# Optimization experiments

Measured on AMD Instinct MI355X. Metric: run time of the kernel, lower is better.

## Reference

```python
import jax, jax.numpy as jnp
import numpy as np

INPUT_SIZE = 128
HID = 64
B, T = 256, 1024

def setup_inputs() -> dict:
    key = jax.random.key(0)
    ks = jax.random.split(key, 12)
    s1 = 1.0 / np.sqrt(HID)
    def u(k, shape):
        return jax.random.uniform(k, shape, jnp.float32, -s1, s1)
    return {
        "x": jax.random.normal(ks[0], (B, T, INPUT_SIZE), jnp.float32),
        "w_ih0": u(ks[1], (4 * HID, INPUT_SIZE)),
        "w_hh0": u(ks[2], (4 * HID, HID)),
        "b_ih0": u(ks[3], (4 * HID,)),
        "b_hh0": u(ks[4], (4 * HID,)),
        "w_ih1": u(ks[5], (4 * HID, HID)),
        "w_hh1": u(ks[6], (4 * HID, HID)),
        "b_ih1": u(ks[7], (4 * HID,)),
        "b_hh1": u(ks[8], (4 * HID,)),
        "w_out": u(ks[9], (1, HID)),
        "b_out": u(ks[10], (1,)),
    }

def _lstm(x, w_ih, w_hh, b_ih, b_hh):
    # x: [B, T, I] -> h sequence [B, T, H]; PyTorch gate order i, f, g, o
    Bb = x.shape[0]
    H = w_hh.shape[1]
    # precompute input contribution for all timesteps (one big GEMM)
    xg = jnp.einsum('bti,gi->btg', x, w_ih) + b_ih + b_hh  # [B, T, 4H]
    def step(carry, g_t):
        h, c = carry
        g = g_t + h @ w_hh.T  # [B, 4H]
        i, f, gg, o = jnp.split(g, 4, axis=-1)
        i = jax.nn.sigmoid(i)
        f = jax.nn.sigmoid(f)
        gg = jnp.tanh(gg)
        o = jax.nn.sigmoid(o)
        c = f * c + i * gg
        h = o * jnp.tanh(c)
        return (h, c), h
    init = (jnp.zeros((Bb, H), x.dtype), jnp.zeros((Bb, H), x.dtype))
    _, hs = jax.lax.scan(step, init, jnp.swapaxes(xg, 0, 1))  # [T, B, H]
    return jnp.swapaxes(hs, 0, 1)

def reference(x, w_ih0, w_hh0, b_ih0, b_hh0, w_ih1, w_hh1, b_ih1, b_hh1, w_out, b_out):
    h1 = _lstm(x, w_ih0, w_hh0, b_ih0, b_hh0)   # [B, T, H]
    h2 = _lstm(h1, w_ih1, w_hh1, b_ih1, b_hh1)  # [B, T, H]
    logits = jnp.einsum('bth,oh->bto', h2, w_out) + b_out  # [B, T, 1]
    return jax.nn.sigmoid(logits)
```

## Files before the change

kernel.cpp:

```cpp
#include <hip/hip_runtime.h>

#define BB 256
#define TT 1024
#define II 128
#define HH 64
#define BT (BB * TT)

typedef _Float16 h2 __attribute__((ext_vector_type(2)));
typedef _Float16 half8 __attribute__((ext_vector_type(8)));
typedef float f32x4 __attribute__((ext_vector_type(4)));
typedef unsigned int uint;
typedef unsigned short ushort;

#define BC(u) __builtin_bit_cast(h2, (uint)(u))
#define MFMA16(a, b, c) __builtin_amdgcn_mfma_f32_16x16x32_f16((a), (b), (c), 0, 0, 0)
#define SIG(v) __builtin_amdgcn_rcpf(1.0f + __expf(-(v)))
#define TNH(v) (1.0f - 2.0f * __builtin_amdgcn_rcpf(1.0f + __expf(2.0f * (v))))

#define BAR() asm volatile("s_waitcnt lgkmcnt(0)\n\ts_barrier" ::: "memory")

__device__ __forceinline__ uint pk2(float a, float b) {
    h2 h; h[0] = (_Float16)a; h[1] = (_Float16)b;
    return __builtin_bit_cast(uint, h);
}

__global__ __launch_bounds__(256)
void xg_mfma(const float* __restrict__ x, const float* __restrict__ w_ih0,
             ushort* __restrict__ xg)
{
    __shared__ __align__(16) _Float16 xt[64][136];
    __shared__ __align__(16) _Float16 wt[128][136];
    const int tid = threadIdx.x, lane = tid & 63, wv = tid >> 6;
    const int bt0 = blockIdx.x * 64;
    {
        const int row = tid >> 2, q = (tid & 3) * 32;
        const float4* src = (const float4*)(x + (size_t)(bt0 + row) * II + q);
        _Float16* dst = &xt[row][q];
        #pragma unroll
        for (int i = 0; i < 8; ++i) {
            float4 v = src[i];
            dst[4*i+0]=(_Float16)v.x; dst[4*i+1]=(_Float16)v.y;
            dst[4*i+2]=(_Float16)v.z; dst[4*i+3]=(_Float16)v.w;
        }
    }
    for (int nh = 0; nh < 2; ++nh) {
        __syncthreads();
        {
            const int n = tid >> 1, kh = (tid & 1) * 64;
            const int flatn = nh * 128 + n;
            const int srcrow = (flatn & 3) * 64 + (flatn >> 2);
            const float4* src = (const float4*)(w_ih0 + (size_t)srcrow * II + kh);
            _Float16* dst = &wt[n][kh];
            #pragma unroll
            for (int i = 0; i < 16; ++i) {
                float4 v = src[i];
                dst[4*i+0]=(_Float16)v.x; dst[4*i+1]=(_Float16)v.y;
                dst[4*i+2]=(_Float16)v.z; dst[4*i+3]=(_Float16)v.w;
            }
        }
        __syncthreads();
        const int m = wv * 16 + (lane & 15);
        const int kf = (lane >> 4) * 8;
        half8 a0 = *(const half8*)&xt[m][ 0 + kf];
        half8 a1 = *(const half8*)&xt[m][32 + kf];
        half8 a2 = *(const half8*)&xt[m][64 + kf];
        half8 a3 = *(const half8*)&xt[m][96 + kf];
        #pragma unroll
        for (int nt = 0; nt < 8; ++nt) {
            const int nloc = nt * 16 + (lane & 15);
            half8 b0 = *(const half8*)&wt[nloc][ 0 + kf];
            half8 b1 = *(const half8*)&wt[nloc][32 + kf];
            half8 b2 = *(const half8*)&wt[nloc][64 + kf];
            half8 b3 = *(const half8*)&wt[nloc][96 + kf];
            f32x4 acc = {0.f, 0.f, 0.f, 0.f};
            acc = MFMA16(a0, b0, acc); acc = MFMA16(a1, b1, acc);
            acc = MFMA16(a2, b2, acc); acc = MFMA16(a3, b3, acc);
            const int colg = nh * 128 + nt * 16 + (lane & 15);
            const int jj = colg >> 2, gg = colg & 3;
            const int r0 = wv * 16 + (lane >> 4) * 4;
            const int bloc = bt0 >> 10;
            const int tb = (bt0 & 1023) + r0;
            ushort* dst = xg + ((size_t)(bloc * 64 + jj) << 12) + gg;
            #pragma unroll
            for (int r = 0; r < 4; ++r) {
                _Float16 hv = (_Float16)acc[r];
                dst[(size_t)(tb + r) * 4] = __builtin_bit_cast(ushort, hv);
            }
        }
    }
}

__global__ __launch_bounds__(192) __attribute__((amdgpu_waves_per_eu(1, 1)))
void lstm2_core(const float* __restrict__ w_hh0,
                const float* __restrict__ b_ih0, const float* __restrict__ b_hh0,
                const float* __restrict__ w_ih1, const float* __restrict__ w_hh1,
                const float* __restrict__ b_ih1, const float* __restrict__ b_hh1,
                const ushort* __restrict__ xg, ushort* __restrict__ h1g)
{
    const int bb = blockIdx.x;
    const int w  = threadIdx.x >> 6;
    const int j  = threadIdx.x & 63;
    const int qq = j >> 4, cc = j & 15;

    __shared__ __align__(16) uint  h0buf[8][32];
    __shared__ __align__(16) uint  h1buf[32];
    __shared__ __align__(16) float zbuf[8][64][4];

    const float* Wsel = (w == 0) ? w_hh0 : (w == 1) ? w_ih1 : w_hh1;
    uint4 Bf[16][2];
    #pragma unroll
    for (int t = 0; t < 16; ++t) {
        const int row = (t & 3) * 64 + (t >> 2) * 16 + cc;
        const float* rp = Wsel + (size_t)row * 64 + qq * 8;
        #pragma unroll
        for (int kh = 0; kh < 2; ++kh) {
            const float* p = rp + kh * 32;
            uint4 v;
            v.x = pk2(p[0], p[1]); v.y = pk2(p[2], p[3]);
            v.z = pk2(p[4], p[5]); v.w = pk2(p[6], p[7]);
            Bf[t][kh] = v;
        }
    }

    float bI = 0.f, bF = 0.f, bG = 0.f, bO = 0.f;
    if (w == 0) {
        bI = b_ih0[j]       + b_hh0[j];
        bF = b_ih0[64 + j]  + b_hh0[64 + j];
        bG = b_ih0[128 + j] + b_hh0[128 + j];
        bO = b_ih0[192 + j] + b_hh0[192 + j];
    } else if (w == 2) {
        bI = b_ih1[j]       + b_hh1[j];
        bF = b_ih1[64 + j]  + b_hh1[64 + j];
        bG = b_ih1[128 + j] + b_hh1[128 + j];
        bO = b_ih1[192 + j] + b_hh1[192 + j];
    }

    float cst = 0.0f;
    const ushort* xb = xg + ((size_t)(bb * 64 + j) << 12);
    ushort* h1b = h1g + (size_t)bb * TT * 64 + j;

    const f32x4 ZR4 = {0.f, 0.f, 0.f, 0.f};
    const int qlo = qq & 1, qhi = qq >> 1;

    half8 af0 = {0,0,0,0,0,0,0,0}, af1 = {0,0,0,0,0,0,0,0};
    f32x4 zr = {0.f, 0.f, 0.f, 0.f};
    uint4 q0 = {0,0,0,0}, q1 = {0,0,0,0};
    if (w == 0) {
        q0 = *(const uint4*)(xb);
        q1 = *(const uint4*)(xb + 8);
    }

#define LDAF(SRC) { const char* hb_ = (const char*)(SRC); \
    af0 = *(const half8*)(hb_ + (qq << 4)); \
    af1 = *(const half8*)(hb_ + 64 + (qq << 4)); }

#define GEMV16(SI, SF, SG, SO) { \
    f32x4 D[16]; \
    _Pragma("unroll") \
    for (int t = 0; t < 16; ++t) { \
        f32x4 d_ = MFMA16(af0, __builtin_bit_cast(half8, Bf[t][0]), ZR4); \
        D[t] = MFMA16(af1, __builtin_bit_cast(half8, Bf[t][1]), d_); } \
    { float a_, b_; \
      a_ = qlo ? D[ 4][0] : D[ 0][0]; b_ = qlo ? D[12][0] : D[ 8][0]; SI = qhi ? b_ : a_; \
      a_ = qlo ? D[ 5][0] : D[ 1][0]; b_ = qlo ? D[13][0] : D[ 9][0]; SF = qhi ? b_ : a_; \
      a_ = qlo ? D[ 6][0] : D[ 2][0]; b_ = qlo ? D[14][0] : D[10][0]; SG = qhi ? b_ : a_; \
      a_ = qlo ? D[ 7][0] : D[ 3][0]; b_ = qlo ? D[15][0] : D[11][0]; SO = qhi ? b_ : a_; } }

#define PSTEP(KK, XLO, XHI) \
    if ((KK) < TT) { \
        float si, sf, sg, so; \
        GEMV16(si, sf, sg, so) \
        h2 xlo = BC(XLO), xhi = BC(XHI); \
        si += bI + (float)xlo[0]; sf += bF + (float)xlo[1]; \
        sg += bG + (float)xhi[0]; so += bO + (float)xhi[1]; \
        float ii = SIG(si), ff = SIG(sf), gg = TNH(sg), oo = SIG(so); \
        cst = fmaf(ff, cst, ii * gg); \
        float hval = oo * TNH(cst); \
        ((_Float16*)&h0buf[(KK) & 7][0])[j] = (_Float16)hval; \
        LDAF(&h0buf[(KK) & 7][0]) \
    }

#define Q1STEP(KK) { const int i_ = (KK); \
    if (i_ >= 3 && i_ < TT + 3) { \
        const int m_ = i_ - 3; \
        float si, sf, sg, so; \
        GEMV16(si, sf, sg, so) \
        f32x4 zv = {si, sf, sg, so}; \
        *(f32x4*)&zbuf[m_ & 7][j][0] = zv; \
    } \
    if (i_ >= 2 && i_ < TT + 2) LDAF(&h0buf[(i_ - 2) & 7][0]) }

#define Q2STEP(KK) { const int i_ = (KK); \
    if (i_ >= 6) { \
        const int m_ = i_ - 6; \
        float si, sf, sg, so; \
        GEMV16(si, sf, sg, so) \
        si += bI + zr[0]; sf += bF + zr[1]; \
        sg += bG + zr[2]; so += bO + zr[3]; \
        float ii = SIG(si), ff = SIG(sf), gg = TNH(sg), oo = SIG(so); \
        cst = fmaf(ff, cst, ii * gg); \
        float hval = oo * TNH(cst); \
        _Float16 hf = (_Float16)hval; \
        ((_Float16*)&h1buf[0])[j] = hf; \
        LDAF(&h1buf[0]) \
        h1b[(size_t)m_ * 64] = __builtin_bit_cast(ushort, hf); \
    } \
    if (i_ >= 5 && i_ < TT + 5) zr = *(const f32x4*)&zbuf[(i_ - 5) & 7][j][0]; }

    for (int k0 = 0; k0 < TT + 6; k0 += 2) {
        if (w == 0) {
            uint4 qn = q1;
            if (k0 + 4 < TT)
                qn = *(const uint4*)(xb + (size_t)(k0 + 4) * 4);
            PSTEP(k0,     q0.x, q0.y)
            PSTEP(k0 + 1, q0.z, q0.w)
            q0 = q1; q1 = qn;
        } else if (w == 1) {
            Q1STEP(k0)
            Q1STEP(k0 + 1)
        } else {
            Q2STEP(k0)
            Q2STEP(k0 + 1)
        }
        BAR();
    }
#undef PSTEP
#undef Q1STEP
#undef Q2STEP
#undef GEMV16
#undef LDAF
}

__global__ __launch_bounds__(256)
void head_gemv(const ushort* __restrict__ h1g, const float* __restrict__ w_out,
               const float* __restrict__ b_out, float* __restrict__ outp)
{
    __shared__ float wsh[64];
    const int tid = threadIdx.x;
    if (tid < 64) wsh[tid] = w_out[tid];
    __syncthreads();
    const int bt = blockIdx.x * 256 + tid;
    const uint4* hp = (const uint4*)(h1g + (size_t)bt * 64);
    float s = 0.0f;
    #pragma unroll
    for (int i = 0; i < 8; ++i) {
        uint4 v = hp[i];
        const float* wp = &wsh[8 * i];
        h2 p;
        p = BC(v.x); s = fmaf((float)p[0], wp[0], s); s = fmaf((float)p[1], wp[1], s);
        p = BC(v.y); s = fmaf((float)p[0], wp[2], s); s = fmaf((float)p[1], wp[3], s);
        p = BC(v.z); s = fmaf((float)p[0], wp[4], s); s = fmaf((float)p[1], wp[5], s);
        p = BC(v.w); s = fmaf((float)p[0], wp[6], s); s = fmaf((float)p[1], wp[7], s);
    }
    outp[bt] = __builtin_amdgcn_rcpf(1.0f + __expf(-(s + b_out[0])));
}

extern "C" void kernel_launch(void* const* d_in, const int* in_sizes, int n_in,
                              void* d_out, int out_size, void* d_ws, size_t ws_size,
                              hipStream_t stream) {
    const float* x     = (const float*)d_in[0];
    const float* w_ih0 = (const float*)d_in[1];
    const float* w_hh0 = (const float*)d_in[2];
    const float* b_ih0 = (const float*)d_in[3];
    const float* b_hh0 = (const float*)d_in[4];
    const float* w_ih1 = (const float*)d_in[5];
    const float* w_hh1 = (const float*)d_in[6];
    const float* b_ih1 = (const float*)d_in[7];
    const float* b_hh1 = (const float*)d_in[8];
    const float* w_out = (const float*)d_in[9];
    const float* b_out = (const float*)d_in[10];
    float* out = (float*)d_out;

    ushort* xg  = (ushort*)d_ws;
    ushort* h1g = (ushort*)((char*)d_ws + (size_t)BT * 256 * 2);

    hipLaunchKernelGGL(xg_mfma, dim3(BT / 64), dim3(256), 0, stream, x, w_ih0, xg);
    hipLaunchKernelGGL(lstm2_core, dim3(BB), dim3(192), 0, stream,
                       w_hh0, b_ih0, b_hh0, w_ih1, w_hh1, b_ih1, b_hh1, xg, h1g);
    hipLaunchKernelGGL(head_gemv, dim3(BT / 256), dim3(256), 0, stream,
                       h1g, w_out, b_out, out);
}
```

Baseline: 758.3 us.

## Fuse layer-0 input projection into recurrent kernel via dedicated producer wave

Removes the separate xg_mfma kernel and its fp16 global xg buffer. A fourth wave in each LSTM block now loads x windows of 16 timesteps and computes the input projection with MFMA against w_ih0 fragments held in LDS. Results go into a double-buffered LDS tile that the layer-0 wave reads each step. This cuts a kernel launch and the global write and read-back of the gate preactivations. In exchange each block carries extra LDS and a fourth wave that must keep pace inside the per-step barrier loop.

```diff
diff --git a/kernel.cpp b/kernel.cpp
--- a/kernel.cpp
+++ b/kernel.cpp
@@ -24,101 +24,55 @@
     return __builtin_bit_cast(uint, h);
 }
 
-__global__ __launch_bounds__(256)
-void xg_mfma(const float* __restrict__ x, const float* __restrict__ w_ih0,
-             ushort* __restrict__ xg)
-{
-    __shared__ __align__(16) _Float16 xt[64][136];
-    __shared__ __align__(16) _Float16 wt[128][136];
-    const int tid = threadIdx.x, lane = tid & 63, wv = tid >> 6;
-    const int bt0 = blockIdx.x * 64;
-    {
-        const int row = tid >> 2, q = (tid & 3) * 32;
-        const float4* src = (const float4*)(x + (size_t)(bt0 + row) * II + q);
-        _Float16* dst = &xt[row][q];
-        #pragma unroll
-        for (int i = 0; i < 8; ++i) {
-            float4 v = src[i];
-            dst[4*i+0]=(_Float16)v.x; dst[4*i+1]=(_Float16)v.y;
-            dst[4*i+2]=(_Float16)v.z; dst[4*i+3]=(_Float16)v.w;
-        }
-    }
-    for (int nh = 0; nh < 2; ++nh) {
-        __syncthreads();
-        {
-            const int n = tid >> 1, kh = (tid & 1) * 64;
-            const int flatn = nh * 128 + n;
-            const int srcrow = (flatn & 3) * 64 + (flatn >> 2);
-            const float4* src = (const float4*)(w_ih0 + (size_t)srcrow * II + kh);
-            _Float16* dst = &wt[n][kh];
-            #pragma unroll
-            for (int i = 0; i < 16; ++i) {
-                float4 v = src[i];
-                dst[4*i+0]=(_Float16)v.x; dst[4*i+1]=(_Float16)v.y;
-                dst[4*i+2]=(_Float16)v.z; dst[4*i+3]=(_Float16)v.w;
-            }
-        }
-        __syncthreads();
-        const int m = wv * 16 + (lane & 15);
-        const int kf = (lane >> 4) * 8;
-        half8 a0 = *(const half8*)&xt[m][ 0 + kf];
-        half8 a1 = *(const half8*)&xt[m][32 + kf];
-        half8 a2 = *(const half8*)&xt[m][64 + kf];
-        half8 a3 = *(const half8*)&xt[m][96 + kf];
-        #pragma unroll
-        for (int nt = 0; nt < 8; ++nt) {
-            const int nloc = nt * 16 + (lane & 15);
-            half8 b0 = *(const half8*)&wt[nloc][ 0 + kf];
-            half8 b1 = *(const half8*)&wt[nloc][32 + kf];
-            half8 b2 = *(const half8*)&wt[nloc][64 + kf];
-            half8 b3 = *(const half8*)&wt[nloc][96 + kf];
-            f32x4 acc = {0.f, 0.f, 0.f, 0.f};
-            acc = MFMA16(a0, b0, acc); acc = MFMA16(a1, b1, acc);
-            acc = MFMA16(a2, b2, acc); acc = MFMA16(a3, b3, acc);
-            const int colg = nh * 128 + nt * 16 + (lane & 15);
-            const int jj = colg >> 2, gg = colg & 3;
-            const int r0 = wv * 16 + (lane >> 4) * 4;
-            const int bloc = bt0 >> 10;
-            const int tb = (bt0 & 1023) + r0;
-            ushort* dst = xg + ((size_t)(bloc * 64 + jj) << 12) + gg;
-            #pragma unroll
-            for (int r = 0; r < 4; ++r) {
-                _Float16 hv = (_Float16)acc[r];
-                dst[(size_t)(tb + r) * 4] = __builtin_bit_cast(ushort, hv);
-            }
-        }
-    }
-}
-
-__global__ __launch_bounds__(192) __attribute__((amdgpu_waves_per_eu(1, 1)))
-void lstm2_core(const float* __restrict__ w_hh0,
+__global__ __launch_bounds__(256) __attribute__((amdgpu_waves_per_eu(1, 1)))
+void lstm2_core(const float* __restrict__ x, const float* __restrict__ w_ih0,
+                const float* __restrict__ w_hh0,
                 const float* __restrict__ b_ih0, const float* __restrict__ b_hh0,
                 const float* __restrict__ w_ih1, const float* __restrict__ w_hh1,
                 const float* __restrict__ b_ih1, const float* __restrict__ b_hh1,
-                const ushort* __restrict__ xg, ushort* __restrict__ h1g)
+                ushort* __restrict__ h1g)
 {
     const int bb = blockIdx.x;
     const int w  = threadIdx.x >> 6;
     const int j  = threadIdx.x & 63;
     const int qq = j >> 4, cc = j & 15;
-
-    __shared__ __align__(16) uint  h0buf[8][32];
-    __shared__ __align__(16) uint  h1buf[32];
-    __shared__ __align__(16) float zbuf[8][64][4];
-
-    const float* Wsel = (w == 0) ? w_hh0 : (w == 1) ? w_ih1 : w_hh1;
-    uint4 Bf[16][2];
-    #pragma unroll
-    for (int t = 0; t < 16; ++t) {
-        const int row = (t & 3) * 64 + (t >> 2) * 16 + cc;
-        const float* rp = Wsel + (size_t)row * 64 + qq * 8;
+    const int j4 = j * 4;
+
+    __shared__ __align__(16) uint   h0buf[8][32];
+    __shared__ __align__(16) uint   h1buf[32];
+    __shared__ __align__(16) float  zbuf[8][64][4];
+    __shared__ __align__(16) ushort xgb[2][16][264];
+    __shared__ __align__(16) uint4  wfrag[16][4][4][16];
+
+    {
         #pragma unroll
-        for (int kh = 0; kh < 2; ++kh) {
-            const float* p = rp + kh * 32;
+        for (int t = 0; t < 16; ++t) {
+            const int flat = t * 16 + cc;
+            const int srcrow = (flat & 3) * 64 + (flat >> 2);
+            const float* p = w_ih0 + (size_t)srcrow * II + w * 32 + qq * 8;
             uint4 v;
             v.x = pk2(p[0], p[1]); v.y = pk2(p[2], p[3]);
             v.z = pk2(p[4], p[5]); v.w = pk2(p[6], p[7]);
-            Bf[t][kh] = v;
+            wfrag[t][w][qq][cc] = v;
+        }
+    }
+    __syncthreads();
+
+    uint4 Bf[16][2];
+    if (w < 3) {
+        const float* Wsel = (w == 0) ? w_hh0 : (w == 1) ? w_ih1 : w_hh1;
+        #pragma unroll
+        for (int t = 0; t < 16; ++t) {
+            const int row = (t & 3) * 64 + (t >> 2) * 16 + cc;
+            const float* rp = Wsel + (size_t)row * 64 + qq * 8;
+            #pragma unroll
+            for (int kh = 0; kh < 2; ++kh) {
+                const float* p = rp + kh * 32;
+                uint4 v;
+                v.x = pk2(p[0], p[1]); v.y = pk2(p[2], p[3]);
+                v.z = pk2(p[4], p[5]); v.w = pk2(p[6], p[7]);
+                Bf[t][kh] = v;
+            }
         }
     }
 
@@ -136,7 +90,7 @@
     }
 
     float cst = 0.0f;
-    const ushort* xb = xg + ((size_t)(bb * 64 + j) << 12);
+    const float* xrow = x + (size_t)bb * TT * II;
     ushort* h1b = h1g + (size_t)bb * TT * 64 + j;
 
     const f32x4 ZR4 = {0.f, 0.f, 0.f, 0.f};
@@ -144,11 +98,50 @@
 
     half8 af0 = {0,0,0,0,0,0,0,0}, af1 = {0,0,0,0,0,0,0,0};
     f32x4 zr = {0.f, 0.f, 0.f, 0.f};
-    uint4 q0 = {0,0,0,0}, q1 = {0,0,0,0};
-    if (w == 0) {
-        q0 = *(const uint4*)(xb);
-        q1 = *(const uint4*)(xb + 8);
-    }
+
+    float4 xr[8];
+    half8 wa0 = {0,0,0,0,0,0,0,0}, wa1 = wa0, wa2 = wa0, wa3 = wa0;
+
+#define XLOAD(WND) if ((WND) < 64) { \
+    const float* xp_ = xrow + (size_t)((WND) * 16 + cc) * II + qq * 8; \
+    xr[0] = *(const float4*)(xp_ +  0); xr[1] = *(const float4*)(xp_ +  4); \
+    xr[2] = *(const float4*)(xp_ + 32); xr[3] = *(const float4*)(xp_ + 36); \
+    xr[4] = *(const float4*)(xp_ + 64); xr[5] = *(const float4*)(xp_ + 68); \
+    xr[6] = *(const float4*)(xp_ + 96); xr[7] = *(const float4*)(xp_ + 100); }
+
+#define MKAF4() { uint4 u_; \
+    u_.x = pk2(xr[0].x, xr[0].y); u_.y = pk2(xr[0].z, xr[0].w); \
+    u_.z = pk2(xr[1].x, xr[1].y); u_.w = pk2(xr[1].z, xr[1].w); \
+    wa0 = __builtin_bit_cast(half8, u_); \
+    u_.x = pk2(xr[2].x, xr[2].y); u_.y = pk2(xr[2].z, xr[2].w); \
+    u_.z = pk2(xr[3].x, xr[3].y); u_.w = pk2(xr[3].z, xr[3].w); \
+    wa1 = __builtin_bit_cast(half8, u_); \
+    u_.x = pk2(xr[4].x, xr[4].y); u_.y = pk2(xr[4].z, xr[4].w); \
+    u_.z = pk2(xr[5].x, xr[5].y); u_.w = pk2(xr[5].z, xr[5].w); \
+    wa2 = __builtin_bit_cast(half8, u_); \
+    u_.x = pk2(xr[6].x, xr[6].y); u_.y = pk2(xr[6].z, xr[6].w); \
+    u_.z = pk2(xr[7].x, xr[7].y); u_.w = pk2(xr[7].z, xr[7].w); \
+    wa3 = __builtin_bit_cast(half8, u_); }
+
+#define WTILE(TILE, BUF) { \
+    f32x4 d_ = ZR4; \
+    d_ = MFMA16(wa0, __builtin_bit_cast(half8, wfrag[TILE][0][qq][cc]), d_); \
+    d_ = MFMA16(wa1, __builtin_bit_cast(half8, wfrag[TILE][1][qq][cc]), d_); \
+    d_ = MFMA16(wa2, __builtin_bit_cast(half8, wfrag[TILE][2][qq][cc]), d_); \
+    d_ = MFMA16(wa3, __builtin_bit_cast(half8, wfrag[TILE][3][qq][cc]), d_); \
+    _Pragma("unroll") \
+    for (int r_ = 0; r_ < 4; ++r_) { \
+        _Float16 hv_ = (_Float16)d_[r_]; \
+        xgb[BUF][qq * 4 + r_][(TILE) * 16 + cc] = __builtin_bit_cast(ushort, hv_); } }
+
+    if (w == 3) {
+        XLOAD(0)
+        MKAF4()
+        #pragma unroll
+        for (int t = 0; t < 16; ++t) WTILE(t, 0)
+        XLOAD(1)
+    }
+    __syncthreads();
 
 #define LDAF(SRC) { const char* hb_ = (const char*)(SRC); \
     af0 = *(const half8*)(hb_ + (qq << 4)); \
@@ -166,11 +159,12 @@
       a_ = qlo ? D[ 6][0] : D[ 2][0]; b_ = qlo ? D[14][0] : D[10][0]; SG = qhi ? b_ : a_; \
       a_ = qlo ? D[ 7][0] : D[ 3][0]; b_ = qlo ? D[15][0] : D[11][0]; SO = qhi ? b_ : a_; } }
 
-#define PSTEP(KK, XLO, XHI) \
+#define PSTEP(KK) \
     if ((KK) < TT) { \
+        const uint2 xcv = *(const uint2*)&xgb[((KK) >> 4) & 1][(KK) & 15][j4]; \
         float si, sf, sg, so; \
         GEMV16(si, sf, sg, so) \
-        h2 xlo = BC(XLO), xhi = BC(XHI); \
+        h2 xlo = BC(xcv.x), xhi = BC(xcv.y); \
         si += bI + (float)xlo[0]; sf += bF + (float)xlo[1]; \
         sg += bG + (float)xhi[0]; so += bO + (float)xhi[1]; \
         float ii = SIG(si), ff = SIG(sf), gg = TNH(sg), oo = SIG(so); \
@@ -209,18 +203,26 @@
 
     for (int k0 = 0; k0 < TT + 6; k0 += 2) {
         if (w == 0) {
-            uint4 qn = q1;
-            if (k0 + 4 < TT)
-                qn = *(const uint4*)(xb + (size_t)(k0 + 4) * 4);
-            PSTEP(k0,     q0.x, q0.y)
-            PSTEP(k0 + 1, q0.z, q0.w)
-            q0 = q1; q1 = qn;
+            PSTEP(k0)
+            PSTEP(k0 + 1)
         } else if (w == 1) {
             Q1STEP(k0)
             Q1STEP(k0 + 1)
-        } else {
+        } else if (w == 2) {
             Q2STEP(k0)
             Q2STEP(k0 + 1)
+        } else {
+            const int s   = (k0 >> 1) & 7;
+            const int wnd = (k0 >> 4) + 1;
+            if (s == 0) {
+                if (wnd < 64) MKAF4()
+                XLOAD(wnd + 1)
+            }
+            if (wnd < 64) {
+                const int buf = wnd & 1;
+                WTILE(2 * s,     buf)
+                WTILE(2 * s + 1, buf)
+            }
         }
         BAR();
     }
@@ -229,6 +231,9 @@
 #undef Q2STEP
 #undef GEMV16
 #undef LDAF
+#undef WTILE
+#undef MKAF4
+#undef XLOAD
 }
 
 __global__ __launch_bounds__(256)
@@ -271,12 +276,11 @@
     const float* b_out = (const float*)d_in[10];
     float* out = (float*)d_out;
 
-    ushort* xg  = (ushort*)d_ws;
-    ushort* h1g = (ushort*)((char*)d_ws + (size_t)BT * 256 * 2);
-
-    hipLaunchKernelGGL(xg_mfma, dim3(BT / 64), dim3(256), 0, stream, x, w_ih0, xg);
-    hipLaunchKernelGGL(lstm2_core, dim3(BB), dim3(192), 0, stream,
-                       w_hh0, b_ih0, b_hh0, w_ih1, w_hh1, b_ih1, b_hh1, xg, h1g);
+    ushort* h1g = (ushort*)d_ws;
+
+    hipLaunchKernelGGL(lstm2_core, dim3(BB), dim3(256), 0, stream,
+                       x, w_ih0, w_hh0, b_ih0, b_hh0,
+                       w_ih1, w_hh1, b_ih1, b_hh1, h1g);
     hipLaunchKernelGGL(head_gemv, dim3(BT / 256), dim3(256), 0, stream,
                        h1g, w_out, b_out, out);
 }
```

After: 800.6 us. 1.06x slower.
